# Optimization experiments

Hardware: AMD Instinct MI355X
Metric: run time of the kernel (lower is better)

The kernel has to match this reference:

```python
import jax, jax.numpy as jnp
import numpy as np

K = 4            # number of modes (init kwarg)
ALPHA = 2000.0   # bandwidth constraint
TAU = 0.0        # dual ascent step (0 -> exact reconstruction slack)
N_ITERS = 20     # fixed ADMM iterations (orig: tol-based while loop, max 500)


def vmd_batch(x):
    # x: [B, C, T] float32 -> (u: [B, C, K, T], omega: [B, C, K])
    B, C, T = x.shape
    T2 = 2 * T
    half = T2 // 2
    # mirror extension (vmdpy): flip first half | signal | flip second half
    f = jnp.concatenate([x[..., :T // 2][..., ::-1], x, x[..., T // 2:][..., ::-1]], axis=-1)  # [B,C,T2]
    t = jnp.arange(1, T2 + 1, dtype=jnp.float32) / T2
    freqs = t - 0.5 - 1.0 / T2                       # [T2], centered frequency axis
    freqs_pos = freqs[half:]                          # [T], positive frequencies
    f_hat = jnp.fft.fftshift(jnp.fft.fft(f, axis=-1), axes=-1).astype(jnp.complex64)
    f_hat_plus = f_hat.at[..., :half].set(0.0)        # keep analytic (positive-freq) part
    # init=1: uniform initial center frequencies
    omega = jnp.broadcast_to((0.5 / K) * jnp.arange(K, dtype=jnp.float32), (B, C, K))
    u_hat = jnp.zeros((B, C, K, T2), dtype=jnp.complex64)
    lam = jnp.zeros((B, C, T2), dtype=jnp.complex64)  # dual variable lambda_hat

    def step(carry, _):
        u_hat, omega, lam = carry
        S = jnp.sum(u_hat, axis=2)                    # running sum of all modes [B,C,T2]
        new_u, new_w = [], []
        for k in range(K):                            # Gauss-Seidel sweep over K modes (K small, unrolled)
            S = S - u_hat[:, :, k]                    # sum of all other modes (updated ones included)
            denom = 1.0 + ALPHA * (freqs[None, None, :] - omega[:, :, k:k + 1]) ** 2
            uk = (f_hat_plus - S + lam / 2.0) / denom # Wiener-filter spectral update [B,C,T2]
            S = S + uk
            p = uk.real[..., half:] ** 2 + uk.imag[..., half:] ** 2  # power on positive freqs [B,C,T]
            wk = jnp.sum(freqs_pos * p, axis=-1) / jnp.sum(p, axis=-1)  # center-frequency re-estimate
            new_u.append(uk)
            new_w.append(wk)
        u_hat = jnp.stack(new_u, axis=2)
        omega = jnp.stack(new_w, axis=-1)
        lam = lam + TAU * (S - f_hat_plus)            # dual ascent (tau=0 -> no-op, kept for fidelity)
        return (u_hat, omega, lam), None

    (u_hat, omega, lam), _ = jax.lax.scan(step, (u_hat, omega, lam), None, length=N_ITERS)

    # reconstruct full conjugate-symmetric spectrum
    pos = u_hat[..., half:]                           # [B,C,K,T]
    full = jnp.zeros((B, C, K, T2), dtype=jnp.complex64)
    full = full.at[..., half:].set(pos)
    full = full.at[..., 1:half + 1].set(jnp.conj(pos)[..., ::-1])  # full[half-j] = conj(pos[j])
    full = full.at[..., 0].set(jnp.conj(full[..., -1]))
    u = jnp.real(jnp.fft.ifft(jnp.fft.ifftshift(full, axes=-1), axis=-1))  # [B,C,K,T2]
    u = u[..., T2 // 4: 3 * T2 // 4]                  # de-mirror: center T samples
    return u, omega


def setup_inputs() -> dict:
    key = jax.random.key(0)
    x = jax.random.normal(key, (16, 8192, 4), dtype=jnp.float32)  # [B, T, C]
    return {"x": x}


def reference(x):
    # module forward: permute [B,T,C] -> [B,C,T], run VMD, return u:[B,K,T,C], omega:[B,K]
    u, omega = vmd_batch(jnp.transpose(x, (0, 2, 1)))
    u = jnp.transpose(u, (0, 2, 3, 1))                # [B,K,T,C]
    omega_b = jnp.mean(omega, axis=1)                 # collapse channel dim -> [B,K]
    return (u, omega_b)
```

## Files before the change

kernel.cpp:

```cpp
#include <hip/hip_runtime.h>


#define HALF      8192
#define NH        8192
#define NTHREADS  1024
#define KMODES    4
#define NITERS    20
#define ALPHA_F   2000.0f
#define SQH       0.70710678118654752440f
#define SENTINEL  0xFFFFFFFFu

typedef __fp16 half2_t __attribute__((ext_vector_type(2)));
typedef float  v2f     __attribute__((ext_vector_type(2)));

__device__ __forceinline__ unsigned bitrev13(unsigned x) { return __brev(x) >> 19; }
__device__ __forceinline__ int pidx(int i) { return i + (i >> 4); }

__device__ __forceinline__ unsigned pack_h2(float a, float b) {
    half2_t h = __builtin_amdgcn_cvt_pkrtz(a, b);
    return __builtin_bit_cast(unsigned, h);
}
__device__ __forceinline__ v2f unpack_h2(unsigned u) {
    half2_t h = __builtin_bit_cast(half2_t, u);
    v2f r; r.x = (float)h.x; r.y = (float)h.y; return r;
}

__device__ __forceinline__ unsigned ic_load(const unsigned* p) {
    return __hip_atomic_load(p, __ATOMIC_RELAXED, __HIP_MEMORY_SCOPE_AGENT);
}
__device__ __forceinline__ void ic_store(unsigned* p, unsigned v) {
    __hip_atomic_store(p, v, __ATOMIC_RELAXED, __HIP_MEMORY_SCOPE_AGENT);
}
__device__ __forceinline__ void store_plain(unsigned* p, unsigned v) {
    asm volatile("global_store_dword %0, %1, off" :: "v"(p), "v"(v) : "memory");
}
__device__ __forceinline__ unsigned load_sc0(const unsigned* p) {
    unsigned r;
    asm volatile("global_load_dword %0, %1, off sc0\n\t"
                 "s_waitcnt vmcnt(0)"
                 : "=v"(r) : "v"(p) : "memory");
    return r;
}

template <int CTRL>
__device__ __forceinline__ float dpp_add_step(float v) {
    int r = __builtin_amdgcn_update_dpp(0, __float_as_int(v), CTRL, 0xf, 0xf, true);
    return v + __int_as_float(r);
}
__device__ __forceinline__ float wave64_sum(float v) {
    v = dpp_add_step<0x111>(v);
    v = dpp_add_step<0x112>(v);
    v = dpp_add_step<0x114>(v);
    v = dpp_add_step<0x118>(v);
    v = dpp_add_step<0x142>(v);
    v = dpp_add_step<0x143>(v);
    return v;
}

__device__ __forceinline__ float2 cmul(float2 a, float wr, float wi) {
    return make_float2(a.x * wr - a.y * wi, a.x * wi + a.y * wr);
}
__device__ __forceinline__ float2 cadd(float2 a, float2 b) {
    return make_float2(a.x + b.x, a.y + b.y);
}
__device__ __forceinline__ float2 csub(float2 a, float2 b) {
    return make_float2(a.x - b.x, a.y - b.y);
}

template <bool INV>
__device__ __forceinline__ void fft_pass8(float2* A, int tid, int t) {
    const int   log2Q = 10 - 3 * t;
    const int   Q     = 1 << log2Q;
    const float invL  = (float)(1 << (3 * t)) * (1.0f / 8192.0f);
    const int j    = tid & (Q - 1);
    const int base = ((tid >> log2Q) << (log2Q + 3)) + j;

    float2 x[8];
    #pragma unroll
    for (int m = 0; m < 8; ++m) x[m] = A[pidx(base + m * Q)];

    float rev = (float)j * invL;
    float w1r = __builtin_amdgcn_cosf(rev);
    float w1i = INV ?  __builtin_amdgcn_sinf(rev)
                    : -__builtin_amdgcn_sinf(rev);
    float w2r = w1r * w1r - w1i * w1i, w2i = 2.0f * w1r * w1i;
    float w4r = w2r * w2r - w2i * w2i, w4i = 2.0f * w2r * w2i;
    float wsr, wsi;
    if (INV) { wsr = SQH * (w1r - w1i); wsi = SQH * (w1r + w1i); }
    else     { wsr = SQH * (w1r + w1i); wsi = SQH * (w1i - w1r); }
    float w1tr = INV ? -w1i : w1i,  w1ti = INV ? w1r : -w1r;
    float wstr = INV ? -wsi : wsi,  wsti = INV ? wsr : -wsr;
    float w2tr = INV ? -w2i : w2i,  w2ti = INV ? w2r : -w2r;

    float2 y0 = cadd(x[0], x[4]), y1 = cadd(x[1], x[5]);
    float2 y2 = cadd(x[2], x[6]), y3 = cadd(x[3], x[7]);
    float2 y4 = cmul(csub(x[0], x[4]), w1r, w1i);
    float2 y5 = cmul(csub(x[1], x[5]), wsr, wsi);
    float2 y6 = cmul(csub(x[2], x[6]), w1tr, w1ti);
    float2 y7 = cmul(csub(x[3], x[7]), wstr, wsti);

    float2 z0 = cadd(y0, y2), z2 = cmul(csub(y0, y2), w2r, w2i);
    float2 z1 = cadd(y1, y3), z3 = cmul(csub(y1, y3), w2tr, w2ti);
    float2 z4 = cadd(y4, y6), z6 = cmul(csub(y4, y6), w2r, w2i);
    float2 z5 = cadd(y5, y7), z7 = cmul(csub(y5, y7), w2tr, w2ti);

    A[pidx(base + 0 * Q)] = cadd(z0, z1);
    A[pidx(base + 1 * Q)] = cmul(csub(z0, z1), w4r, w4i);
    A[pidx(base + 2 * Q)] = cadd(z2, z3);
    A[pidx(base + 3 * Q)] = cmul(csub(z2, z3), w4r, w4i);
    A[pidx(base + 4 * Q)] = cadd(z4, z5);
    A[pidx(base + 5 * Q)] = cmul(csub(z4, z5), w4r, w4i);
    A[pidx(base + 6 * Q)] = cadd(z6, z7);
    A[pidx(base + 7 * Q)] = cmul(csub(z6, z7), w4r, w4i);
}

__device__ __forceinline__ void fft_last2(float2* A, int tid) {
    #pragma unroll
    for (int u = 0; u < 4; ++u) {
        int t  = tid + u * NTHREADS;
        int i0 = 2 * t, i1 = 2 * t + 1;
        float2 a = A[pidx(i0)], b = A[pidx(i1)];
        A[pidx(i0)] = make_float2(a.x + b.x, a.y + b.y);
        A[pidx(i1)] = make_float2(a.x - b.x, a.y - b.y);
    }
}

__device__ __forceinline__ int mirror_t(int i) {
    if (i < 4096)       return 4095 - i;
    else if (i < 12288) return i - 4096;
    else                return 20479 - i;
}

__global__ __launch_bounds__(NTHREADS) void vmd_fused(
    const float* __restrict__ x, unsigned* __restrict__ ws_u,
    unsigned* __restrict__ ws_omega, unsigned* __restrict__ ws_partf,
    unsigned* __restrict__ ws_parts, unsigned* __restrict__ ws_udone,
    float* __restrict__ out)
{
    __shared__ float2 A[NH + (NH >> 4)];
    const int tid = threadIdx.x;
    const int bid = blockIdx.x;
    const int r8  = bid & 7;
    const int q   = (bid >> 3) & 3;
    const int a8  = bid >> 5;
    const int ch  = a8 * 8 + r8;
    const int b   = ch >> 2, c = ch & 3;
    const float* xb = x + (size_t)b * 8192 * 4 + c;

    for (int m = tid; m < NH; m += NTHREADS) {
        float re = xb[(size_t)mirror_t(2 * m) * 4];
        float im = xb[(size_t)mirror_t(2 * m + 1) * 4];
        A[pidx(m)] = make_float2(re, im);
    }
    __syncthreads();

    for (int t = 0; t < 4; ++t) {
        fft_pass8<false>(A, tid, t);
        __syncthreads();
    }
    fft_last2(A, tid);
    __syncthreads();

    v2f R[2];
    #pragma unroll
    for (int u = 0; u < 2; ++u) {
        int j  = (q << 11) + tid + u * NTHREADS;
        float2 z1 = A[pidx((int)bitrev13((unsigned)j))];
        float2 z2 = A[pidx((int)bitrev13((unsigned)((NH - j) & (NH - 1))))];
        float ex = 0.5f * (z1.x + z2.x);
        float ey = 0.5f * (z1.y - z2.y);
        float dx = 0.5f * (z1.x - z2.x);
        float dy = 0.5f * (z1.y + z2.y);
        float rev = (float)j * (1.0f / 16384.0f);
        float wr = __builtin_amdgcn_cosf(rev);
        float wi = -__builtin_amdgcn_sinf(rev);
        R[u].x = ex + wr * dy + wi * dx;
        R[u].y = ey + wi * dy - wr * dx;
    }
    __syncthreads();

    v2f Up[KMODES][2];
    #pragma unroll
    for (int u = 0; u < 2; ++u)
        #pragma unroll
        for (int k = 0; k < KMODES; ++k) { Up[k][u].x = 0.f; Up[k][u].y = 0.f; }

    const float f0 = (float)((q << 11) + tid) * (1.0f / 16384.0f);
    float omg[KMODES] = {0.0f, 0.125f, 0.25f, 0.375f};

    float* red = (float*)A;
    const int lane = tid & 63, wid = tid >> 6;

    for (int it = 0; it < NITERS; ++it) {
        v2f nd[KMODES];
        #pragma unroll
        for (int k = 0; k < KMODES; ++k) { nd[k].x = 0.f; nd[k].y = 0.f; }
        #pragma unroll
        for (int u = 0; u < 2; ++u) {
            const float fru = f0 + (float)u * 0.0625f;
            v2f fv; fv.x = fru; fv.y = 1.0f;
            #pragma unroll
            for (int k = 0; k < KMODES; ++k) {
                float d   = fru - omg[k];
                float dnm = fmaf(ALPHA_F * d, d, 1.0f);
                float rcp = __builtin_amdgcn_rcpf(dnm);
                v2f uo  = Up[k][u];
                v2f nm  = R[u] + uo;
                v2f un  = nm * rcp;
                R[u]    = nm - un;
                Up[k][u] = un;
                float p = fmaf(un.x, un.x, un.y * un.y);
                nd[k]   = fv * p + nd[k];
            }
        }
        float num[KMODES], den[KMODES];
        #pragma unroll
        for (int m = 0; m < KMODES; ++m) {
            num[m] = wave64_sum(nd[m].x);
            den[m] = wave64_sum(nd[m].y);
        }
        float* redb = red + (it & 1) * 144;
        if (lane == 63) {
            float4* r4 = (float4*)&redb[wid * 8];
            r4[0] = make_float4(num[0], num[1], num[2], num[3]);
            r4[1] = make_float4(den[0], den[1], den[2], den[3]);
        }
        __syncthreads();
        const bool last_it = (it == NITERS - 1);
        unsigned* ppf = ws_partf + (((size_t)it * 64 + ch) << 5);
        unsigned* pps = ws_parts + (((size_t)it * 64 + ch) << 5);
        if (wid == 0) {
            float v = redb[lane] + redb[lane + 64];
            v += __int_as_float(__builtin_amdgcn_ds_swizzle(__float_as_int(v), 0x201F));
            v += __int_as_float(__builtin_amdgcn_ds_swizzle(__float_as_int(v), 0x401F));
            v += __int_as_float(__builtin_amdgcn_ds_bpermute((lane ^ 32) << 2,
                                                             __float_as_int(v)));
            if (lane < 8) {
                unsigned bits = __float_as_uint(v);
                store_plain(ppf + (q << 3) + lane, bits);
                ic_store(pps + (q << 3) + lane, bits);
            }
            if (!last_it || q == 0) {
                float t = 0.0f;
                if (lane < 32) {
                    unsigned w;
                    for (;;) {
                        w = load_sc0(ppf + lane);
                        if (w != SENTINEL) break;
                        w = ic_load(pps + lane);
                        if (w != SENTINEL) break;
                        __builtin_amdgcn_s_sleep(1);
                    }
                    t = __uint_as_float(w);
                }
                t += __int_as_float(__builtin_amdgcn_ds_swizzle(__float_as_int(t), 0x201F));
                t += __int_as_float(__builtin_amdgcn_ds_swizzle(__float_as_int(t), 0x401F));
                if (!last_it) {
                    if (lane < 8) redb[128 + lane] = t;
                } else {
                    #pragma unroll
                    for (int m = 0; m < KMODES; ++m) {
                        float nm_ = __int_as_float(__builtin_amdgcn_readlane(__float_as_int(t), m));
                        float dn_ = __int_as_float(__builtin_amdgcn_readlane(__float_as_int(t), m + 4));
                        omg[m] = nm_ * __builtin_amdgcn_rcpf(dn_);
                    }
                }
            }
        }
        if (!last_it) {
            __syncthreads();
            #pragma unroll
            for (int m = 0; m < KMODES; ++m) {
                float nm_ = redb[128 + m];
                float dn_ = redb[128 + m + 4];
                omg[m] = nm_ * __builtin_amdgcn_rcpf(dn_);
            }
        }
    }

    #pragma unroll
    for (int k = 0; k < KMODES; ++k) {
        unsigned* dst = ws_u + (size_t)(ch * KMODES + k) * HALF + (q << 11);
        #pragma unroll
        for (int u = 0; u < 2; ++u)
            ic_store(dst + tid + u * NTHREADS, pack_h2(Up[k][u].x, Up[k][u].y));
    }
    if (q == 0 && tid < KMODES)
        ic_store(ws_omega + ch * KMODES + tid, __float_as_uint(omg[tid]));
    asm volatile("s_waitcnt vmcnt(0)" ::: "memory");
    __syncthreads();
    if (tid == 0)
        ic_store(ws_udone + (ch << 2) + q, 0u);

    const int g2  = bid & 63;
    const int c2  = bid >> 6;
    const int b2  = g2 >> 2, k2 = g2 & 3;
    const int ch2 = b2 * 4 + c2;
    const unsigned* pos = ws_u + (size_t)(ch2 * KMODES + k2) * HALF;

    if (bid == 0 && tid < 64) {
        int bb = tid >> 2, kk = tid & 3;
        float s = 0.f;
        #pragma unroll
        for (int cc = 0; cc < 4; ++cc) {
            const unsigned* p = ws_omega + ((bb * 4 + cc) << 2) + kk;
            unsigned w;
            for (;;) {
                w = ic_load(p);
                if (w != SENTINEL) break;
                __builtin_amdgcn_s_sleep(1);
            }
            s += __uint_as_float(w);
        }
        out[2097152 + tid] = 0.25f * s;
    }

    if (tid < 4) {
        const unsigned* p = ws_udone + (ch2 << 2) + tid;
        for (;;) {
            unsigned w = ic_load(p);
            if (w != SENTINEL) break;
            __builtin_amdgcn_s_sleep(1);
        }
    }
    __syncthreads();

    {
        unsigned wj[8], wh[8];
        #pragma unroll
        for (int uu = 0; uu < 8; ++uu) {
            int j = tid + uu * NTHREADS;
            wj[uu] = ic_load(pos + j);
            wh[uu] = ic_load(pos + (j ? (HALF - j) : (HALF - 1)));
        }
        #pragma unroll
        for (int uu = 0; uu < 8; ++uu) {
            int j = tid + uu * NTHREADS;
            v2f pj = unpack_h2(wj[uu]);
            v2f ph = unpack_h2(wh[uu]);
            float gjx = pj.x, gjy = (j == 0) ? -pj.y : pj.y;
            float ghx = ph.x, ghy = -ph.y;
            float ex = 0.5f * (gjx + ghx), ey = 0.5f * (gjy + ghy);
            float dx = 0.5f * (gjx - ghx), dy = 0.5f * (gjy - ghy);
            float rev = (float)j * (1.0f / 16384.0f);
            float wr = __builtin_amdgcn_cosf(rev);
            float wi = __builtin_amdgcn_sinf(rev);
            float ox = dx * wr - dy * wi;
            float oy = dx * wi + dy * wr;
            A[pidx(j)] = make_float2(ex - oy, ey + ox);
        }
    }
    __syncthreads();

    for (int t = 0; t < 4; ++t) {
        fft_pass8<true>(A, tid, t);
        __syncthreads();
    }
    fft_last2(A, tid);
    __syncthreads();

    float* outp = out + (size_t)(b2 * 4 + k2) * 8192 * 4 + c2;
    for (int m = 2048 + tid; m < 6144; m += NTHREADS) {
        float2 z = A[pidx((int)bitrev13((unsigned)m))];
        int t0 = 2 * m - 4096;
        outp[(size_t)t0 * 4]       = z.x * (1.0f / 8192.0f);
        outp[(size_t)(t0 + 1) * 4] = z.y * (1.0f / 8192.0f);
    }
}

extern "C" void kernel_launch(void* const* d_in, const int* in_sizes, int n_in,
                              void* d_out, int out_size, void* d_ws, size_t ws_size,
                              hipStream_t stream)
{
    (void)in_sizes; (void)n_in; (void)out_size; (void)ws_size;
    const float* x = (const float*)d_in[0];
    float* out = (float*)d_out;

    unsigned* ws_u     = (unsigned*)d_ws;
    unsigned* ws_omega = (unsigned*)((char*)d_ws + (size_t)64 * 4 * HALF * 4);
    unsigned* ws_partf = ws_omega + 256;
    unsigned* ws_parts = ws_partf + (size_t)NITERS * 64 * 32;
    unsigned* ws_udone = ws_parts + (size_t)NITERS * 64 * 32;

    hipMemsetAsync(ws_omega, 0xFF,
                   (size_t)(256 + 2 * NITERS * 64 * 32 + 256) * 4, stream);
    vmd_fused<<<256, NTHREADS, 0, stream>>>(x, ws_u, ws_omega, ws_partf,
                                            ws_parts, ws_udone, out);
}
```

Baseline: 83.46 us.

## Split forward FFT across four cooperating blocks via decimation and global exchange

Previously each of the four blocks assigned to a channel computed the full 8192-point forward FFT redundantly. Now each block computes one 2048-point sub-FFT of a decimated slice of the input, publishes it to global workspace, and raises a flag. Each block then waits on the flags of its three peers and recombines the four sub-FFTs with radix-4 twiddles into its own spectrum slice. This removes redundant FFT work but adds a cross-block spin-wait and an extra global round trip, and it relies on all 256 blocks being resident at the same time.

```diff
diff --git a/kernel.cpp b/kernel.cpp
--- a/kernel.cpp
+++ b/kernel.cpp
@@ -14,6 +14,7 @@
 typedef float  v2f     __attribute__((ext_vector_type(2)));
 
 __device__ __forceinline__ unsigned bitrev13(unsigned x) { return __brev(x) >> 19; }
+__device__ __forceinline__ unsigned bitrev11(unsigned x) { return __brev(x) >> 21; }
 __device__ __forceinline__ int pidx(int i) { return i + (i >> 4); }
 
 __device__ __forceinline__ unsigned pack_h2(float a, float b) {
@@ -29,6 +30,12 @@
     return __hip_atomic_load(p, __ATOMIC_RELAXED, __HIP_MEMORY_SCOPE_AGENT);
 }
 __device__ __forceinline__ void ic_store(unsigned* p, unsigned v) {
+    __hip_atomic_store(p, v, __ATOMIC_RELAXED, __HIP_MEMORY_SCOPE_AGENT);
+}
+__device__ __forceinline__ unsigned long long ic_load64(const unsigned long long* p) {
+    return __hip_atomic_load(p, __ATOMIC_RELAXED, __HIP_MEMORY_SCOPE_AGENT);
+}
+__device__ __forceinline__ void ic_store64(unsigned long long* p, unsigned long long v) {
     __hip_atomic_store(p, v, __ATOMIC_RELAXED, __HIP_MEMORY_SCOPE_AGENT);
 }
 __device__ __forceinline__ void store_plain(unsigned* p, unsigned v) {
@@ -68,12 +75,10 @@
 }
 
 template <bool INV>
-__device__ __forceinline__ void fft_pass8(float2* A, int tid, int t) {
-    const int   log2Q = 10 - 3 * t;
-    const int   Q     = 1 << log2Q;
-    const float invL  = (float)(1 << (3 * t)) * (1.0f / 8192.0f);
-    const int j    = tid & (Q - 1);
-    const int base = ((tid >> log2Q) << (log2Q + 3)) + j;
+__device__ __forceinline__ void fft_pass8_g(float2* A, int bf, int log2Q, float invL) {
+    const int Q    = 1 << log2Q;
+    const int j    = bf & (Q - 1);
+    const int base = ((bf >> log2Q) << (log2Q + 3)) + j;
 
     float2 x[8];
     #pragma unroll
@@ -113,6 +118,10 @@
     A[pidx(base + 6 * Q)] = cadd(z6, z7);
     A[pidx(base + 7 * Q)] = cmul(csub(z6, z7), w4r, w4i);
 }
+template <bool INV>
+__device__ __forceinline__ void fft_pass8(float2* A, int tid, int t) {
+    fft_pass8_g<INV>(A, tid, 10 - 3 * t, (float)(1 << (3 * t)) * (1.0f / 8192.0f));
+}
 
 __device__ __forceinline__ void fft_last2(float2* A, int tid) {
     #pragma unroll
@@ -125,6 +134,20 @@
     }
 }
 
+__device__ __forceinline__ void fft2048_last4(float2* A, int g) {
+    int i0 = 4 * g;
+    float2 a0 = A[pidx(i0)], a1 = A[pidx(i0 + 1)];
+    float2 a2 = A[pidx(i0 + 2)], a3 = A[pidx(i0 + 3)];
+    float2 b0 = cadd(a0, a2), b1 = cadd(a1, a3);
+    float2 b2 = csub(a0, a2);
+    float2 d  = csub(a1, a3);
+    float2 b3 = make_float2(d.y, -d.x);
+    A[pidx(i0)]     = cadd(b0, b1);
+    A[pidx(i0 + 1)] = csub(b0, b1);
+    A[pidx(i0 + 2)] = cadd(b2, b3);
+    A[pidx(i0 + 3)] = csub(b2, b3);
+}
+
 __device__ __forceinline__ int mirror_t(int i) {
     if (i < 4096)       return 4095 - i;
     else if (i < 12288) return i - 4096;
@@ -135,6 +158,7 @@
     const float* __restrict__ x, unsigned* __restrict__ ws_u,
     unsigned* __restrict__ ws_omega, unsigned* __restrict__ ws_partf,
     unsigned* __restrict__ ws_parts, unsigned* __restrict__ ws_udone,
+    unsigned* __restrict__ ws_yflag, unsigned long long* __restrict__ ws_Y,
     float* __restrict__ out)
 {
     __shared__ float2 A[NH + (NH >> 4)];
@@ -147,35 +171,90 @@
     const int b   = ch >> 2, c = ch & 3;
     const float* xb = x + (size_t)b * 8192 * 4 + c;
 
-    for (int m = tid; m < NH; m += NTHREADS) {
-        float re = xb[(size_t)mirror_t(2 * m) * 4];
-        float im = xb[(size_t)mirror_t(2 * m + 1) * 4];
+    for (int m = tid; m < 2048; m += NTHREADS) {
+        int i0 = 8 * m + 2 * q;
+        float re = xb[(size_t)mirror_t(i0) * 4];
+        float im = xb[(size_t)mirror_t(i0 + 1) * 4];
         A[pidx(m)] = make_float2(re, im);
     }
     __syncthreads();
-
-    for (int t = 0; t < 4; ++t) {
-        fft_pass8<false>(A, tid, t);
+    for (int t = 0; t < 3; ++t) {
+        if (tid < 256)
+            fft_pass8_g<false>(A, tid, 8 - 3 * t,
+                               (float)(1 << (3 * t)) * (1.0f / 2048.0f));
         __syncthreads();
     }
-    fft_last2(A, tid);
+    if (tid < 512) fft2048_last4(A, tid);
+    __syncthreads();
+
+    {
+        unsigned long long* ydst = ws_Y + ((size_t)ch * 4 + q) * 2048;
+        for (int n = tid; n < 2048; n += NTHREADS) {
+            float2 v = A[pidx((int)bitrev11((unsigned)n))];
+            ic_store64(ydst + n, __builtin_bit_cast(unsigned long long, v));
+        }
+    }
+    asm volatile("s_waitcnt vmcnt(0)" ::: "memory");
+    __syncthreads();
+    if (tid == 0) ic_store(ws_yflag + ch * 4 + q, 0u);
+    if (tid < 4) {
+        const unsigned* p = ws_yflag + ch * 4 + tid;
+        for (;;) {
+            unsigned w = ic_load(p);
+            if (w != SENTINEL) break;
+            __builtin_amdgcn_s_sleep(1);
+        }
+    }
+    __syncthreads();
+
+    {
+        const unsigned long long* ysrc = ws_Y + (size_t)ch * 8192;
+        unsigned long long yv[8];
+        #pragma unroll
+        for (int w = 0; w < 8; ++w)
+            yv[w] = ic_load64(ysrc + tid + w * NTHREADS);
+        #pragma unroll
+        for (int w = 0; w < 8; ++w)
+            A[pidx(tid + w * NTHREADS)] = __builtin_bit_cast(float2, yv[w]);
+    }
     __syncthreads();
 
     v2f R[2];
     #pragma unroll
     for (int u = 0; u < 2; ++u) {
-        int j  = (q << 11) + tid + u * NTHREADS;
-        float2 z1 = A[pidx((int)bitrev13((unsigned)j))];
-        float2 z2 = A[pidx((int)bitrev13((unsigned)((NH - j) & (NH - 1))))];
-        float ex = 0.5f * (z1.x + z2.x);
-        float ey = 0.5f * (z1.y - z2.y);
-        float dx = 0.5f * (z1.x - z2.x);
-        float dy = 0.5f * (z1.y + z2.y);
-        float rev = (float)j * (1.0f / 16384.0f);
+        int jp  = tid + u * NTHREADS;
+        int j   = (q << 11) + jp;
+        int j2p = (2048 - jp) & 2047;
+        float2 y0 = A[pidx(jp)];
+        float2 y1 = A[pidx(2048 + jp)];
+        float2 y2 = A[pidx(4096 + jp)];
+        float2 y3 = A[pidx(6144 + jp)];
+        float2 h0 = A[pidx(j2p)];
+        float2 h1 = A[pidx(2048 + j2p)];
+        float2 h2 = A[pidx(4096 + j2p)];
+        float2 h3 = A[pidx(6144 + j2p)];
+        float rev = (float)j * (1.0f / 8192.0f);
         float wr = __builtin_amdgcn_cosf(rev);
         float wi = -__builtin_amdgcn_sinf(rev);
-        R[u].x = ex + wr * dy + wi * dx;
-        R[u].y = ey + wi * dy - wr * dx;
+        float w2r = wr * wr - wi * wi, w2i = 2.0f * wr * wi;
+        float w3r = w2r * wr - w2i * wi, w3i = w2r * wi + w2i * wr;
+        float2 zj = y0;
+        zj.x += y1.x * wr  - y1.y * wi;  zj.y += y1.x * wi  + y1.y * wr;
+        zj.x += y2.x * w2r - y2.y * w2i; zj.y += y2.x * w2i + y2.y * w2r;
+        zj.x += y3.x * w3r - y3.y * w3i; zj.y += y3.x * w3i + y3.y * w3r;
+        float2 zh = h0;
+        zh.x += h1.x * wr  + h1.y * wi;  zh.y += -h1.x * wi  + h1.y * wr;
+        zh.x += h2.x * w2r + h2.y * w2i; zh.y += -h2.x * w2i + h2.y * w2r;
+        zh.x += h3.x * w3r + h3.y * w3i; zh.y += -h3.x * w3i + h3.y * w3r;
+        float ex = 0.5f * (zj.x + zh.x);
+        float ey = 0.5f * (zj.y - zh.y);
+        float dx = 0.5f * (zj.x - zh.x);
+        float dy = 0.5f * (zj.y + zh.y);
+        float rev2 = (float)j * (1.0f / 16384.0f);
+        float ur = __builtin_amdgcn_cosf(rev2);
+        float ui = -__builtin_amdgcn_sinf(rev2);
+        R[u].x = ex + ur * dy + ui * dx;
+        R[u].y = ey + ui * dy - ur * dx;
     }
     __syncthreads();
 
@@ -381,9 +460,12 @@
     unsigned* ws_partf = ws_omega + 256;
     unsigned* ws_parts = ws_partf + (size_t)NITERS * 64 * 32;
     unsigned* ws_udone = ws_parts + (size_t)NITERS * 64 * 32;
+    unsigned* ws_yflag = ws_udone + 256;
+    unsigned long long* ws_Y = (unsigned long long*)(ws_yflag + 256);
 
     hipMemsetAsync(ws_omega, 0xFF,
-                   (size_t)(256 + 2 * NITERS * 64 * 32 + 256) * 4, stream);
+                   (size_t)(256 + 2 * NITERS * 64 * 32 + 256 + 256) * 4, stream);
     vmd_fused<<<256, NTHREADS, 0, stream>>>(x, ws_u, ws_omega, ws_partf,
-                                            ws_parts, ws_udone, out);
-}
+                                            ws_parts, ws_udone, ws_yflag,
+                                            ws_Y, out);
+}
```

Measured after the change: 79.79 us. 4.4% less time.
